# Optimization experiments

Hardware: AMD Instinct MI355X
Metric: run time of the kernel (lower is better)

## Reference

```python
import jax, jax.numpy as jnp
import numpy as np

B, N, DIM, H, DH = 8, 1024, 1024, 16, 64

def setup_inputs() -> dict:
    key = jax.random.key(0)
    ks = jax.random.split(key, 6)
    return {
        'x': jax.random.normal(ks[0], (B, N, DIM), dtype=jnp.float32),
        'freqs': jax.random.normal(ks[1], (1, N, DH), dtype=jnp.float32),
        'bias': jax.random.normal(ks[2], (1, N, DH), dtype=jnp.float32),
        'ln_gamma': jnp.ones((DIM,), jnp.float32),
        'ln_beta': jnp.zeros((DIM,), jnp.float32),
        'w_qk': jax.random.normal(ks[3], (DIM, 2 * H * DH), dtype=jnp.float32) * (DIM ** -0.5),
        'w_v': jax.random.normal(ks[4], (DIM, H * DH), dtype=jnp.float32) * (DIM ** -0.5),
        'w_out': jax.random.normal(ks[5], (H * DH, DIM), dtype=jnp.float32) * ((H * DH) ** -0.5),
        'b_out': jnp.zeros((DIM,), jnp.float32),
    }

def _apply_polar(t, freqs):
    # t: [b,h,n,d]; freqs: [1,n,d] broadcast over b,h. Output doubles last dim.
    t = jax.nn.softplus(t)
    return jnp.concatenate((t * jnp.cos(freqs), t * jnp.sin(freqs)), axis=-1)

def reference(x, freqs, bias, ln_gamma, ln_beta, w_qk, w_v, w_out, b_out):
    eps = 1e-5
    mu = jnp.mean(x, axis=-1, keepdims=True)
    var = jnp.var(x, axis=-1, keepdims=True)
    xn = (x - mu) * jax.lax.rsqrt(var + eps) * ln_gamma + ln_beta
    qk = jnp.einsum('bnd,de->bne', xn, w_qk)
    q, k = jnp.split(qk, 2, axis=-1)
    v = jnp.einsum('bnd,de->bne', xn, w_v)
    split_heads = lambda t: t.reshape(B, N, H, DH).transpose(0, 2, 1, 3)
    q, k, v = split_heads(q), split_heads(k), split_heads(v)
    q = _apply_polar(q, freqs)          # [b,h,n,2*DH]
    k = _apply_polar(k, freqs + bias)   # [b,h,n,2*DH]
    scale = DH ** -0.5
    dots = jnp.einsum('bhnd,bhmd->bhnm', q, k) * scale
    attn = jax.nn.softmax(dots, axis=-1)
    out = jnp.einsum('bhnm,bhmd->bhnd', attn, v)
    out = out.transpose(0, 2, 1, 3).reshape(B, N, H * DH)
    return jnp.einsum('bne,ed->bnd', out, w_out) + b_out
```

## Files before the change

kernel.cpp:

```cpp
#include <hip/hip_runtime.h>
#include <cmath>

using f16   = _Float16;
using f16x2 = __attribute__((ext_vector_type(2))) _Float16;
using f16x4 = __attribute__((ext_vector_type(4))) _Float16;
using f16x8 = __attribute__((ext_vector_type(8))) _Float16;
using f32x4 = __attribute__((ext_vector_type(4))) float;

#define DEV __device__ __forceinline__

constexpr int Bb  = 8;
constexpr int Nn  = 1024;
constexpr int DIM = 1024;
constexpr int Hh  = 16;
constexpr int DH  = 64;
constexpr int EQKV = 3072;

DEV void async16(const f16* g, f16* l) {
  __builtin_amdgcn_global_load_lds(
      (const __attribute__((address_space(1))) void*)g,
      (__attribute__((address_space(3))) void*)l, 16, 0, 0);
}

DEV float softplusf(float x) {
  return fmaxf(x, 0.f) + __logf(1.f + __expf(-fabsf(x)));
}

template <int CTRL>
DEV float dpp_mov(float x) {
  return __builtin_bit_cast(float,
      __builtin_amdgcn_update_dpp(__builtin_bit_cast(int, x), __builtin_bit_cast(int, x),
                                  CTRL, 0xf, 0xf, false));
}
DEV float rmax16(float x) {
  x = fmaxf(x, dpp_mov<0x121>(x));
  x = fmaxf(x, dpp_mov<0x122>(x));
  x = fmaxf(x, dpp_mov<0x124>(x));
  x = fmaxf(x, dpp_mov<0x128>(x));
  return x;
}
DEV float rsum16(float x) {
  x += dpp_mov<0x121>(x);
  x += dpp_mov<0x122>(x);
  x += dpp_mov<0x124>(x);
  x += dpp_mov<0x128>(x);
  return x;
}

__global__ __launch_bounds__(256) void transpose_cvt(const float* __restrict__ src,
                                                     f16* __restrict__ dst,
                                                     int rows, int cols) {
  __shared__ float tile[32][33];
  int t = threadIdx.x, tx = t & 31, ty = t >> 5;
  int c0 = blockIdx.x * 32, r0 = blockIdx.y * 32;
#pragma unroll
  for (int j = 0; j < 32; j += 8)
    tile[ty + j][tx] = src[(size_t)(r0 + ty + j) * cols + c0 + tx];
  __syncthreads();
#pragma unroll
  for (int j = 0; j < 32; j += 8)
    dst[(size_t)(c0 + ty + j) * rows + r0 + tx] = (f16)tile[tx][ty + j];
}

__global__ __launch_bounds__(256) void ln_kernel(const float* __restrict__ x,
                                                 const float* __restrict__ gamma,
                                                 const float* __restrict__ beta,
                                                 f16* __restrict__ xn) {
  int row = blockIdx.x;
  int t = threadIdx.x;
  const float4* xr = (const float4*)(x + (size_t)row * DIM);
  float4 v = xr[t];
  float s  = v.x + v.y + v.z + v.w;
  float s2 = v.x * v.x + v.y * v.y + v.z * v.z + v.w * v.w;
#pragma unroll
  for (int off = 32; off; off >>= 1) {
    s  += __shfl_xor(s,  off, 64);
    s2 += __shfl_xor(s2, off, 64);
  }
  __shared__ float red[8];
  int wv = t >> 6, lane = t & 63;
  if (lane == 0) { red[wv] = s; red[4 + wv] = s2; }
  __syncthreads();
  s  = red[0] + red[1] + red[2] + red[3];
  s2 = red[4] + red[5] + red[6] + red[7];
  float mu  = s * (1.f / DIM);
  float var = s2 * (1.f / DIM) - mu * mu;
  float rs  = rsqrtf(var + 1e-5f);
  float4 g = ((const float4*)gamma)[t];
  float4 bb = ((const float4*)beta)[t];
  f16x4 o;
  o[0] = (f16)((v.x - mu) * rs * g.x + bb.x);
  o[1] = (f16)((v.y - mu) * rs * g.y + bb.y);
  o[2] = (f16)((v.z - mu) * rs * g.z + bb.z);
  o[3] = (f16)((v.w - mu) * rs * g.w + bb.w);
  ((f16x4*)(xn + (size_t)row * DIM))[t] = o;
}

template <bool FP32OUT>
__global__ __launch_bounds__(256) void gemm_bt(const f16* __restrict__ A,
                                               const f16* __restrict__ Bt,
                                               void* __restrict__ Cv,
                                               const float* __restrict__ bias,
                                               int M, int K, int E) {
  __shared__ f16 lA[128 * 32];
  __shared__ f16 lB[128 * 32];
  int tid  = threadIdx.x;
  int lane = tid & 63;
  int wv   = __builtin_amdgcn_readfirstlane(tid >> 6);
  int nbe  = E >> 7;
  int bm = blockIdx.x / nbe, be = blockIdx.x % nbe;
  size_t m0 = (size_t)bm * 128, e0 = (size_t)be * 128;
  int wm = (wv & 1) * 64, we = (wv >> 1) * 64;
  int lm = lane & 15, q = lane >> 4;

  f32x4 acc[4][4] = {};

  int row_s[2], cg_s[2];
#pragma unroll
  for (int r = 0; r < 2; ++r) {
    int s = r * 256 + tid;
    row_s[r] = s >> 2;
    cg_s[r]  = (s & 3) ^ ((row_s[r] >> 1) & 3);
  }
  const f16* pa[4];
  const f16* pb[4];
#pragma unroll
  for (int i = 0; i < 4; ++i) {
    int ra = wm + i * 16 + lm;
    pa[i] = lA + ra * 32 + (q ^ ((ra >> 1) & 3)) * 8;
    int rb = we + i * 16 + lm;
    pb[i] = lB + rb * 32 + (q ^ ((rb >> 1) & 3)) * 8;
  }

  for (int k0 = 0; k0 < K; k0 += 32) {
#pragma unroll
    for (int r = 0; r < 2; ++r) {
      const f16* ga = A  + (m0 + row_s[r]) * K + k0 + cg_s[r] * 8;
      const f16* gb = Bt + (e0 + row_s[r]) * K + k0 + cg_s[r] * 8;
      async16(ga, lA + (r * 256 + wv * 64) * 8);
      async16(gb, lB + (r * 256 + wv * 64) * 8);
    }
    __syncthreads();
    f16x8 af[4], bf[4];
#pragma unroll
    for (int i = 0; i < 4; ++i) {
      af[i] = *(const f16x8*)pa[i];
      bf[i] = *(const f16x8*)pb[i];
    }
#pragma unroll
    for (int i = 0; i < 4; ++i)
#pragma unroll
      for (int j = 0; j < 4; ++j)
        acc[i][j] = __builtin_amdgcn_mfma_f32_16x16x32_f16(af[i], bf[j], acc[i][j], 0, 0, 0);
    __syncthreads();
  }

#pragma unroll
  for (int i = 0; i < 4; ++i) {
    size_t mbase = m0 + wm + i * 16 + q * 4;
#pragma unroll
    for (int j = 0; j < 4; ++j) {
      size_t e = e0 + we + j * 16 + lm;
#pragma unroll
      for (int g = 0; g < 4; ++g) {
        float val = acc[i][j][g];
        if (FP32OUT)
          ((float*)Cv)[(mbase + g) * (size_t)E + e] = val + bias[e];
        else
          ((f16*)Cv)[(mbase + g) * (size_t)E + e] = (f16)val;
      }
    }
  }
}

__global__ __launch_bounds__(256) void polar_kernel(const f16* __restrict__ qkv,
                                                    const float* __restrict__ freqs,
                                                    const float* __restrict__ fbias,
                                                    f16* __restrict__ Qp,
                                                    f16* __restrict__ Kp,
                                                    f16* __restrict__ Vt) {
  __shared__ f16 vt[64 * 66];
  int tid = threadIdx.x;
  int bx = blockIdx.x;
  int nt = bx & 15, bh = bx >> 4;
  int b = bh >> 4, h = bh & 15;
  size_t tok0 = (size_t)b * Nn + nt * 64;
  int n0 = nt * 64;
  constexpr float kScale = 0.125f;
#pragma unroll
  for (int i = 0; i < 8; ++i) {
    int e2 = tid + i * 256;
    int nl = e2 >> 5, dp = (e2 & 31) * 2;
    size_t src = (tok0 + nl) * EQKV + h * 64 + dp;
    f16x2 q2 = *(const f16x2*)(qkv + src);
    f16x2 k2 = *(const f16x2*)(qkv + src + 1024);
    f16x2 v2 = *(const f16x2*)(qkv + src + 2048);
    int fidx = (n0 + nl) * 64 + dp;
    float2 f2  = *(const float2*)(freqs + fidx);
    float2 fb2 = *(const float2*)(fbias + fidx);
    f16x2 qc, qs, kc, ksn;
#pragma unroll
    for (int u = 0; u < 2; ++u) {
      float fq = u ? f2.y : f2.x;
      float fk = fq + (u ? fb2.y : fb2.x);
      float spq = softplusf((float)q2[u]) * kScale;
      float spk = softplusf((float)k2[u]);
      float snq, csq, snk, csk;
      __sincosf(fq, &snq, &csq);
      __sincosf(fk, &snk, &csk);
      qc[u]  = (f16)(spq * csq);
      qs[u]  = (f16)(spq * snq);
      kc[u]  = (f16)(spk * csk);
      ksn[u] = (f16)(spk * snk);
    }
    size_t dst = ((size_t)bh * Nn + n0 + nl) * 128 + dp;
    *(f16x2*)(Qp + dst)      = qc;
    *(f16x2*)(Qp + dst + 64) = qs;
    *(f16x2*)(Kp + dst)      = kc;
    *(f16x2*)(Kp + dst + 64) = ksn;
    vt[dp * 66 + nl]       = v2[0];
    vt[(dp + 1) * 66 + nl] = v2[1];
  }
  __syncthreads();
#pragma unroll
  for (int i = 0; i < 16; ++i) {
    int e = tid + i * 256;
    int d = e >> 6, nl = e & 63;
    Vt[((size_t)bh * 64 + d) * Nn + n0 + nl] = vt[d * 66 + nl];
  }
}

constexpr int AK0 = 0;
constexpr int AK1 = 8192;
constexpr int AV0 = 16384;
constexpr int AV1 = 20480;
constexpr int APB = 24576;

__global__ __launch_bounds__(512, 4) void attn_kernel(const f16* __restrict__ Qp,
                                                      const f16* __restrict__ Kp,
                                                      const f16* __restrict__ Vt,
                                                      f16* __restrict__ attout) {
  __shared__ f16 smem[28672];

  int tid = threadIdx.x, lane = tid & 63;
  int wv = __builtin_amdgcn_readfirstlane(tid >> 6);
  int lm = lane & 15, q = lane >> 4;
  int bx = blockIdx.x;
  int bh = (bx & 7) | ((bx >> 6) << 3);
  int qt = (bx >> 3) & 7;
  const f16* Kbase = Kp + (size_t)bh * Nn * 128;
  const f16* Vbase = Vt + (size_t)bh * 64 * Nn;

#pragma unroll
  for (int i = 0; i < 2; ++i) {
    int s = i * 512 + tid;
    int r = s >> 4, c = s & 15;
    int g = c ^ (r & 15);
    async16(Kbase + (size_t)r * 128 + g * 8, smem + AK0 + (i * 512 + wv * 64) * 8);
  }
  {
    int r = tid >> 3, c = tid & 7;
    int g = c ^ (r & 7);
    async16(Vbase + (size_t)r * Nn + g * 8, smem + AV0 + (wv * 64) * 8);
  }

  f16x8 qf[4];
  {
    const f16* Qb = Qp + ((size_t)bh * Nn + qt * 128 + wv * 16 + lm) * 128;
#pragma unroll
    for (int ks = 0; ks < 4; ++ks)
      qf[ks] = *(const f16x8*)(Qb + ks * 32 + q * 8);
  }

  f32x4 O[4] = {};
  float mrow[4], lrow[4];
#pragma unroll
  for (int g = 0; g < 4; ++g) { mrow[g] = -INFINITY; lrow[g] = 0.f; }
  f16* sP = smem + APB + wv * 512;

  for (int kt = 0; kt < 16; ++kt) {
    __syncthreads();

    if (kt < 15) {
      f16* nK = smem + ((kt & 1) ? AK0 : AK1);
      f16* nV = smem + ((kt & 1) ? AV0 : AV1);
#pragma unroll
      for (int i = 0; i < 2; ++i) {
        int s = i * 512 + tid;
        int r = s >> 4, c = s & 15;
        int g = c ^ (r & 15);
        async16(Kbase + (size_t)((kt + 1) * 64 + r) * 128 + g * 8, nK + (i * 512 + wv * 64) * 8);
      }
      {
        int r = tid >> 3, c = tid & 7;
        int g = c ^ (r & 7);
        async16(Vbase + (size_t)r * Nn + (kt + 1) * 64 + g * 8, nV + (wv * 64) * 8);
      }
    }
    const f16* sK = smem + ((kt & 1) ? AK1 : AK0);
    const f16* sV = smem + ((kt & 1) ? AV1 : AV0);

    f32x4 S[4] = {};
#pragma unroll
    for (int nt = 0; nt < 4; ++nt) {
      f16x8 kf[4];
#pragma unroll
      for (int ks = 0; ks < 4; ++ks)
        kf[ks] = *(const f16x8*)(sK + (nt * 16 + lm) * 128 + (((ks * 4 + q) ^ lm) * 8));
#pragma unroll
      for (int ks = 0; ks < 4; ++ks)
        S[nt] = __builtin_amdgcn_mfma_f32_16x16x32_f16(qf[ks], kf[ks], S[nt], 0, 0, 0);
    }

#pragma unroll
    for (int g = 0; g < 4; ++g) {
      float mx = fmaxf(fmaxf(S[0][g], S[1][g]), fmaxf(S[2][g], S[3][g]));
      mx = rmax16(mx);
      float mn = fmaxf(mrow[g], mx);
      float alpha = __expf(mrow[g] - mn);
      mrow[g] = mn;
      float rs = 0.f;
#pragma unroll
      for (int nt = 0; nt < 4; ++nt) {
        float p = __expf(S[nt][g] - mn);
        S[nt][g] = p;
        rs += p;
      }
      rs = rsum16(rs);
      lrow[g] = lrow[g] * alpha + rs;
#pragma unroll
      for (int nt = 0; nt < 4; ++nt) O[nt][g] *= alpha;
    }

#pragma unroll
    for (int half = 0; half < 2; ++half) {
      __asm__ __volatile__("" ::: "memory");
#pragma unroll
      for (int ntl = 0; ntl < 2; ++ntl) {
        int nt = half * 2 + ntl;
#pragma unroll
        for (int g = 0; g < 4; ++g) {
          int rl = q * 4 + g;
          int ch = (ntl * 2 + (lm >> 3)) ^ q;
          sP[rl * 32 + ch * 8 + (lm & 7)] = (f16)S[nt][g];
        }
      }
      __asm__ __volatile__("" ::: "memory");
      f16x8 pf = *(const f16x8*)(sP + lm * 32 + ((q ^ ((lm >> 2) & 3)) * 8));
#pragma unroll
      for (int nto = 0; nto < 4; ++nto) {
        int row = nto * 16 + lm;
        f16x8 vf = *(const f16x8*)(sV + row * 64 + (((half * 4 + q) ^ (row & 7)) * 8));
        O[nto] = __builtin_amdgcn_mfma_f32_16x16x32_f16(pf, vf, O[nto], 0, 0, 0);
      }
    }
  }

  int b = bh >> 4, h = bh & 15;
  size_t tok0 = (size_t)b * Nn + qt * 128 + wv * 16;
#pragma unroll
  for (int g = 0; g < 4; ++g) {
    size_t token = tok0 + q * 4 + g;
    float inv = 1.f / lrow[g];
#pragma unroll
    for (int nto = 0; nto < 4; ++nto)
      attout[token * (size_t)(Hh * DH) + h * 64 + nto * 16 + lm] =
          (f16)(O[nto][g] * inv);
  }
}

extern "C" void kernel_launch(void* const* d_in, const int* in_sizes, int n_in,
                              void* d_out, int out_size, void* d_ws, size_t ws_size,
                              hipStream_t stream) {
  const float* x     = (const float*)d_in[0];
  const float* freqs = (const float*)d_in[1];
  const float* fbias = (const float*)d_in[2];
  const float* gamma = (const float*)d_in[3];
  const float* beta  = (const float*)d_in[4];
  const float* w_qk  = (const float*)d_in[5];
  const float* w_v   = (const float*)d_in[6];
  const float* w_out = (const float*)d_in[7];
  const float* b_out = (const float*)d_in[8];
  float* out = (float*)d_out;

  const size_t T = (size_t)Bb * Nn;
  f16* WqkvT = (f16*)d_ws;
  f16* WoutT = WqkvT + (size_t)EQKV * DIM;
  f16* Xn    = WoutT + (size_t)DIM * DIM;
  f16* QKV   = Xn + T * DIM;
  f16* AttO  = QKV + T * EQKV;
  f16* Qp    = AttO + T * DIM;
  f16* Kp    = Qp + (size_t)128 * Nn * 128;
  f16* Vt    = Kp + (size_t)128 * Nn * 128;

  transpose_cvt<<<dim3(2048 / 32, 1024 / 32), 256, 0, stream>>>(w_qk, WqkvT, DIM, 2048);
  transpose_cvt<<<dim3(1024 / 32, 1024 / 32), 256, 0, stream>>>(w_v, WqkvT + (size_t)2048 * DIM, DIM, 1024);
  transpose_cvt<<<dim3(1024 / 32, 1024 / 32), 256, 0, stream>>>(w_out, WoutT, DIM, DIM);

  ln_kernel<<<(int)T, 256, 0, stream>>>(x, gamma, beta, Xn);

  gemm_bt<false><<<(int)(T / 128) * (EQKV / 128), 256, 0, stream>>>(
      Xn, WqkvT, (void*)QKV, nullptr, (int)T, DIM, EQKV);

  polar_kernel<<<Bb * Hh * (Nn / 64), 256, 0, stream>>>(QKV, freqs, fbias, Qp, Kp, Vt);

  attn_kernel<<<Bb * Hh * (Nn / 128), 512, 0, stream>>>(Qp, Kp, Vt, AttO);

  gemm_bt<true><<<(int)(T / 128) * (DIM / 128), 256, 0, stream>>>(
      AttO, WoutT, (void*)out, b_out, (int)T, DIM, DIM);
}
```

Measured before the change: 326.7 us.

## Compute transposed S in attention so P feeds PV MFMA from registers

The QK^T MFMA operands are swapped so each lane holds one query row's scores across keys. The softmax row max and sum then become cross-lane shuffles, and the P fragments can be converted to f16 and passed directly as the B operand of 16x16x16 MFMAs against V. This removes the per-wave LDS staging buffer for P and its stores and loads. The shared memory saved lets occupancy hints rise from 4 to 6 blocks. The trade is using the smaller-K MFMA instruction (twice as many PV MFMAs) and 8-byte V reads instead of 16-byte ones.

```diff
diff --git a/kernel.cpp b/kernel.cpp
--- a/kernel.cpp
+++ b/kernel.cpp
@@ -24,27 +24,6 @@
 
 DEV float softplusf(float x) {
   return fmaxf(x, 0.f) + __logf(1.f + __expf(-fabsf(x)));
-}
-
-template <int CTRL>
-DEV float dpp_mov(float x) {
-  return __builtin_bit_cast(float,
-      __builtin_amdgcn_update_dpp(__builtin_bit_cast(int, x), __builtin_bit_cast(int, x),
-                                  CTRL, 0xf, 0xf, false));
-}
-DEV float rmax16(float x) {
-  x = fmaxf(x, dpp_mov<0x121>(x));
-  x = fmaxf(x, dpp_mov<0x122>(x));
-  x = fmaxf(x, dpp_mov<0x124>(x));
-  x = fmaxf(x, dpp_mov<0x128>(x));
-  return x;
-}
-DEV float rsum16(float x) {
-  x += dpp_mov<0x121>(x);
-  x += dpp_mov<0x122>(x);
-  x += dpp_mov<0x124>(x);
-  x += dpp_mov<0x128>(x);
-  return x;
 }
 
 __global__ __launch_bounds__(256) void transpose_cvt(const float* __restrict__ src,
@@ -234,13 +213,12 @@
 constexpr int AK1 = 8192;
 constexpr int AV0 = 16384;
 constexpr int AV1 = 20480;
-constexpr int APB = 24576;
-
-__global__ __launch_bounds__(512, 4) void attn_kernel(const f16* __restrict__ Qp,
+
+__global__ __launch_bounds__(512, 6) void attn_kernel(const f16* __restrict__ Qp,
                                                       const f16* __restrict__ Kp,
                                                       const f16* __restrict__ Vt,
                                                       f16* __restrict__ attout) {
-  __shared__ f16 smem[28672];
+  __shared__ f16 smem[24576];
 
   int tid = threadIdx.x, lane = tid & 63;
   int wv = __builtin_amdgcn_readfirstlane(tid >> 6);
@@ -273,10 +251,7 @@
   }
 
   f32x4 O[4] = {};
-  float mrow[4], lrow[4];
-#pragma unroll
-  for (int g = 0; g < 4; ++g) { mrow[g] = -INFINITY; lrow[g] = 0.f; }
-  f16* sP = smem + APB + wv * 512;
+  float mrow = -INFINITY, lrow = 0.f;
 
   for (int kt = 0; kt < 16; ++kt) {
     __syncthreads();
@@ -309,63 +284,63 @@
         kf[ks] = *(const f16x8*)(sK + (nt * 16 + lm) * 128 + (((ks * 4 + q) ^ lm) * 8));
 #pragma unroll
       for (int ks = 0; ks < 4; ++ks)
-        S[nt] = __builtin_amdgcn_mfma_f32_16x16x32_f16(qf[ks], kf[ks], S[nt], 0, 0, 0);
-    }
-
-#pragma unroll
-    for (int g = 0; g < 4; ++g) {
-      float mx = fmaxf(fmaxf(S[0][g], S[1][g]), fmaxf(S[2][g], S[3][g]));
-      mx = rmax16(mx);
-      float mn = fmaxf(mrow[g], mx);
-      float alpha = __expf(mrow[g] - mn);
-      mrow[g] = mn;
-      float rs = 0.f;
-#pragma unroll
-      for (int nt = 0; nt < 4; ++nt) {
+        S[nt] = __builtin_amdgcn_mfma_f32_16x16x32_f16(kf[ks], qf[ks], S[nt], 0, 0, 0);
+    }
+
+    float mx = -INFINITY;
+#pragma unroll
+    for (int nt = 0; nt < 4; ++nt)
+#pragma unroll
+      for (int g = 0; g < 4; ++g) mx = fmaxf(mx, S[nt][g]);
+    mx = fmaxf(mx, __shfl_xor(mx, 16, 64));
+    mx = fmaxf(mx, __shfl_xor(mx, 32, 64));
+    float mn = fmaxf(mrow, mx);
+    float alpha = __expf(mrow - mn);
+    mrow = mn;
+    float rs = 0.f;
+    f16x4 pf[4];
+#pragma unroll
+    for (int nt = 0; nt < 4; ++nt) {
+#pragma unroll
+      for (int g = 0; g < 4; ++g) {
         float p = __expf(S[nt][g] - mn);
         S[nt][g] = p;
         rs += p;
       }
-      rs = rsum16(rs);
-      lrow[g] = lrow[g] * alpha + rs;
-#pragma unroll
-      for (int nt = 0; nt < 4; ++nt) O[nt][g] *= alpha;
-    }
-
-#pragma unroll
-    for (int half = 0; half < 2; ++half) {
-      __asm__ __volatile__("" ::: "memory");
-#pragma unroll
-      for (int ntl = 0; ntl < 2; ++ntl) {
-        int nt = half * 2 + ntl;
-#pragma unroll
-        for (int g = 0; g < 4; ++g) {
-          int rl = q * 4 + g;
-          int ch = (ntl * 2 + (lm >> 3)) ^ q;
-          sP[rl * 32 + ch * 8 + (lm & 7)] = (f16)S[nt][g];
-        }
-      }
-      __asm__ __volatile__("" ::: "memory");
-      f16x8 pf = *(const f16x8*)(sP + lm * 32 + ((q ^ ((lm >> 2) & 3)) * 8));
-#pragma unroll
-      for (int nto = 0; nto < 4; ++nto) {
-        int row = nto * 16 + lm;
-        f16x8 vf = *(const f16x8*)(sV + row * 64 + (((half * 4 + q) ^ (row & 7)) * 8));
-        O[nto] = __builtin_amdgcn_mfma_f32_16x16x32_f16(pf, vf, O[nto], 0, 0, 0);
+      pf[nt][0] = (f16)S[nt][0];
+      pf[nt][1] = (f16)S[nt][1];
+      pf[nt][2] = (f16)S[nt][2];
+      pf[nt][3] = (f16)S[nt][3];
+    }
+    rs += __shfl_xor(rs, 16, 64);
+    rs += __shfl_xor(rs, 32, 64);
+    lrow = lrow * alpha + rs;
+#pragma unroll
+    for (int nto = 0; nto < 4; ++nto)
+#pragma unroll
+      for (int g = 0; g < 4; ++g) O[nto][g] *= alpha;
+
+#pragma unroll
+    for (int nto = 0; nto < 4; ++nto) {
+      int r = nto * 16 + lm;
+#pragma unroll
+      for (int nt = 0; nt < 4; ++nt) {
+        int c16 = (nt * 2 + (q >> 1)) ^ (r & 7);
+        f16x4 vf = *(const f16x4*)(sV + r * 64 + c16 * 8 + (q & 1) * 4);
+        O[nto] = __builtin_amdgcn_mfma_f32_16x16x16f16(vf, pf[nt], O[nto], 0, 0, 0);
       }
     }
   }
 
   int b = bh >> 4, h = bh & 15;
-  size_t tok0 = (size_t)b * Nn + qt * 128 + wv * 16;
-#pragma unroll
-  for (int g = 0; g < 4; ++g) {
-    size_t token = tok0 + q * 4 + g;
-    float inv = 1.f / lrow[g];
-#pragma unroll
-    for (int nto = 0; nto < 4; ++nto)
-      attout[token * (size_t)(Hh * DH) + h * 64 + nto * 16 + lm] =
-          (f16)(O[nto][g] * inv);
+  size_t token = (size_t)b * Nn + qt * 128 + wv * 16 + lm;
+  float inv = 1.f / lrow;
+#pragma unroll
+  for (int nto = 0; nto < 4; ++nto) {
+    f16x4 o4;
+#pragma unroll
+    for (int g = 0; g < 4; ++g) o4[g] = (f16)(O[nto][g] * inv);
+    *(f16x4*)(attout + token * (size_t)(Hh * DH) + h * 64 + nto * 16 + q * 4) = o4;
   }
 }
 
```

Measured after the change: 315.9 us. -3.3%, faster.
